# Performance work log

Measured on AMD Instinct MI355X. Metric: run time of the kernel, lower is better.

## Reference

```python
import jax, jax.numpy as jnp
import numpy as np

N_STATE = 1024
N_HEAD = 16
HEAD_DIM = N_STATE // N_HEAD


def setup_inputs() -> dict:
    key = jax.random.key(0)
    ks = jax.random.split(key, 8)
    B, S = 8, 1500
    x = jax.random.normal(ks[0], (B, S, N_STATE), dtype=jnp.float32)
    # additive causal mask (0 on/below diagonal, -inf above), broadcast over B,H
    neg = jnp.float32(-1e9)
    mask = jnp.where(jnp.tril(jnp.ones((S, S), dtype=bool)), 0.0, neg).astype(jnp.float32)
    s = 0.02
    Wq = jax.random.normal(ks[1], (N_STATE, N_STATE), dtype=jnp.float32) * s
    bq = jnp.zeros((N_STATE,), dtype=jnp.float32)
    Wk = jax.random.normal(ks[2], (N_STATE, N_STATE), dtype=jnp.float32) * s
    Wv = jax.random.normal(ks[3], (N_STATE, N_STATE), dtype=jnp.float32) * s
    bv = jnp.zeros((N_STATE,), dtype=jnp.float32)
    Wo = jax.random.normal(ks[4], (N_STATE, N_STATE), dtype=jnp.float32) * s
    bo = jnp.zeros((N_STATE,), dtype=jnp.float32)
    return {"x": x, "mask": mask, "Wq": Wq, "bq": bq, "Wk": Wk, "Wv": Wv, "bv": bv, "Wo": Wo, "bo": bo}


def reference(x, mask, Wq, bq, Wk, Wv, bv, Wo, bo):
    B, S, _ = x.shape
    # linear projections (torch Linear: x @ W^T + b); W stored as [out, in]
    q = x @ Wq.T + bq
    k = x @ Wk.T
    v = x @ Wv.T + bv
    # [B, H, S, D]
    q = q.reshape(B, S, N_HEAD, HEAD_DIM).transpose(0, 2, 1, 3)
    k = k.reshape(B, S, N_HEAD, HEAD_DIM).transpose(0, 2, 1, 3)
    v = v.reshape(B, S, N_HEAD, HEAD_DIM).transpose(0, 2, 1, 3)
    scale = 1.0 / np.sqrt(HEAD_DIM).astype(np.float32)
    scores = jnp.einsum('bhqd,bhkd->bhqk', q, k) * scale + mask
    attn = jax.nn.softmax(scores, axis=-1)
    out = jnp.einsum('bhqk,bhkd->bhqd', attn, v)
    out = out.transpose(0, 2, 1, 3).reshape(B, S, N_STATE)
    return out @ Wo.T + bo
```

## Files before the change

### kernel.cpp

```cpp
#include <hip/hip_runtime.h>
#include <hip/hip_bf16.h>

#define N_STATE 1024
#define N_HEAD  16
#define D_HEAD  64
#define BATCH   8
#define SEQ     1500
#define ROWS    (BATCH*SEQ)
#define SVP     1536
#define MTILES  94

#define BM 128
#define BN 128
#define BK 32

typedef __bf16 bf16x8 __attribute__((ext_vector_type(8)));
typedef __bf16 bf16x4 __attribute__((ext_vector_type(4)));
typedef float  f32x4  __attribute__((ext_vector_type(4)));

__device__ __forceinline__ f32x4 mfma16(bf16x8 a, bf16x8 b, f32x4 c) {
  return __builtin_amdgcn_mfma_f32_16x16x32_bf16(a, b, c, 0, 0, 0);
}

__device__ __forceinline__ void gl_lds16(const void* g, void* l) {
  __builtin_amdgcn_global_load_lds(
      (const __attribute__((address_space(1))) unsigned int*)g,
      (__attribute__((address_space(3))) unsigned int*)l, 16, 0, 0);
}

__global__ __launch_bounds__(256)
void cvt_all(const float* __restrict__ x,  const float* __restrict__ wq,
             const float* __restrict__ wk, const float* __restrict__ wv,
             const float* __restrict__ wo,
             __bf16* __restrict__ xb, __bf16* __restrict__ wb)
{
  const int which = blockIdx.y;
  const float* src;
  __bf16* dst;
  size_t n;
  if (which == 0) { src = x; dst = xb; n = (size_t)ROWS * N_STATE; }
  else {
    src = (which == 1) ? wq : (which == 2) ? wk : (which == 3) ? wv : wo;
    dst = wb + (size_t)(which - 1) * N_STATE * N_STATE;
    n = (size_t)N_STATE * N_STATE;
  }
  const size_t stride = (size_t)gridDim.x * 256 * 4;
  for (size_t i = ((size_t)blockIdx.x * 256 + threadIdx.x) * 4; i < n; i += stride) {
    const f32x4 v = *(const f32x4*)(src + i);
    bf16x4 c; c[0]=(__bf16)v[0]; c[1]=(__bf16)v[1]; c[2]=(__bf16)v[2]; c[3]=(__bf16)v[3];
    *(bf16x4*)(dst + i) = c;
  }
}

__global__ __launch_bounds__(256)
void qkv_fast(const __bf16* __restrict__ xb, const __bf16* __restrict__ wb,
              const float* __restrict__ bq, const float* __restrict__ bv,
              __bf16* __restrict__ q_ws, __bf16* __restrict__ k_ws,
              __bf16* __restrict__ vt_ws)
{
  const int xcd = blockIdx.x & 7;
  const int jj  = blockIdx.x >> 3;
  const int nt  = jj & 7;
  const int mt  = (jj >> 3) * 8 + xcd;
  if (mt >= MTILES) return;

  __shared__ __bf16 lA[BM * BK];
  __shared__ __bf16 lB[BN * BK];
  const int which = blockIdx.z;
  const __bf16* W = wb + (size_t)which * N_STATE * N_STATE;

  const int tid = threadIdx.x;
  const int lane = tid & 63, wave = tid >> 6;
  const int l15 = lane & 15, quad = lane >> 4;
  const int wr = wave >> 1, wc = wave & 1;

  f32x4 acc[4][4] = {};

  for (int k0 = 0; k0 < N_STATE; k0 += BK) {
#pragma unroll
    for (int t = 0; t < 2; ++t) {
      const int c = wave * 2 + t;
      const int s = c * 64 + lane;
      const int row = s >> 2;
      const int sw  = (lane & 3) ^ ((row >> 1) & 3);
      const int ga = min(mt * BM + row, ROWS - 1);
      gl_lds16(xb + (size_t)ga * N_STATE + k0 + sw * 8, (__bf16*)lA + c * 512);
      const int gb = nt * BN + row;
      gl_lds16(W + (size_t)gb * N_STATE + k0 + sw * 8, (__bf16*)lB + c * 512);
    }
    __syncthreads();
    bf16x8 af[4], bfr[4];
#pragma unroll
    for (int i = 0; i < 4; ++i) {
      const int ra = wr * 64 + i * 16 + l15;
      const int rb = wc * 64 + i * 16 + l15;
      af[i]  = *(const bf16x8*)&lA[ra * BK + ((quad ^ ((ra >> 1) & 3)) * 8)];
      bfr[i] = *(const bf16x8*)&lB[rb * BK + ((quad ^ ((rb >> 1) & 3)) * 8)];
    }
    if (which != 2) {
#pragma unroll
      for (int i = 0; i < 4; ++i)
#pragma unroll
        for (int j = 0; j < 4; ++j)
          acc[i][j] = mfma16(af[i], bfr[j], acc[i][j]);
    } else {
#pragma unroll
      for (int i = 0; i < 4; ++i)
#pragma unroll
        for (int j = 0; j < 4; ++j)
          acc[i][j] = mfma16(bfr[j], af[i], acc[i][j]);
    }
    __syncthreads();
  }

  if (which != 2) {
#pragma unroll
    for (int i = 0; i < 4; ++i) {
      const int mrow = mt * BM + wr * 64 + i * 16 + quad * 4;
#pragma unroll
      for (int j = 0; j < 4; ++j) {
        const int col = nt * BN + wc * 64 + j * 16 + l15;
        const int h = col >> 6, d = col & 63;
        const float badd = (which == 0) ? bq[col] : 0.0f;
        __bf16* dst = (which == 0) ? q_ws : k_ws;
#pragma unroll
        for (int r = 0; r < 4; ++r) {
          const int row = mrow + r;
          if (row < ROWS) {
            const int b = row / SEQ, s = row % SEQ;
            dst[(((size_t)(b * N_HEAD + h)) * SEQ + s) * D_HEAD + d] =
                (__bf16)(acc[i][j][r] + badd);
          }
        }
      }
    }
  } else {
#pragma unroll
    for (int i = 0; i < 4; ++i) {
      const int sg = mt * BM + wr * 64 + i * 16 + l15;
      const bool valid = sg < ROWS;
      const int b = sg / SEQ, srow = sg % SEQ;
#pragma unroll
      for (int j = 0; j < 4; ++j) {
        const int dbase = nt * BN + wc * 64 + j * 16 + quad * 4;
#pragma unroll
        for (int r = 0; r < 4; ++r) {
          const int d = dbase + r;
          const int h = d >> 6, dd = d & 63;
          if (valid)
            vt_ws[(((size_t)(b * N_HEAD + h)) * D_HEAD + dd) * SVP + srow] =
                (__bf16)(acc[i][j][r] + bv[d]);
        }
      }
    }
  }
}

__global__ __launch_bounds__(256)
void out_fast(const __bf16* __restrict__ a_in, const __bf16* __restrict__ wob,
              const float* __restrict__ bo, float* __restrict__ out)
{
  const int xcd = blockIdx.x & 7;
  const int jj  = blockIdx.x >> 3;
  const int nt  = jj & 7;
  const int mt  = (jj >> 3) * 8 + xcd;
  if (mt >= MTILES) return;

  __shared__ __bf16 lA[BM * BK];
  __shared__ __bf16 lB[BN * BK];
  const int tid = threadIdx.x;
  const int lane = tid & 63, wave = tid >> 6;
  const int l15 = lane & 15, quad = lane >> 4;
  const int wr = wave >> 1, wc = wave & 1;

  f32x4 acc[4][4] = {};

  for (int k0 = 0; k0 < N_STATE; k0 += BK) {
#pragma unroll
    for (int t = 0; t < 2; ++t) {
      const int c = wave * 2 + t;
      const int s = c * 64 + lane;
      const int row = s >> 2;
      const int sw  = (lane & 3) ^ ((row >> 1) & 3);
      const int ga = min(mt * BM + row, ROWS - 1);
      gl_lds16(a_in + (size_t)ga * N_STATE + k0 + sw * 8, (__bf16*)lA + c * 512);
      const int gb = nt * BN + row;
      gl_lds16(wob + (size_t)gb * N_STATE + k0 + sw * 8, (__bf16*)lB + c * 512);
    }
    __syncthreads();
    bf16x8 af[4], bfr[4];
#pragma unroll
    for (int i = 0; i < 4; ++i) {
      const int ra = wr * 64 + i * 16 + l15;
      const int rb = wc * 64 + i * 16 + l15;
      af[i]  = *(const bf16x8*)&lA[ra * BK + ((quad ^ ((ra >> 1) & 3)) * 8)];
      bfr[i] = *(const bf16x8*)&lB[rb * BK + ((quad ^ ((rb >> 1) & 3)) * 8)];
    }
#pragma unroll
    for (int i = 0; i < 4; ++i)
#pragma unroll
      for (int j = 0; j < 4; ++j)
        acc[i][j] = mfma16(af[i], bfr[j], acc[i][j]);
    __syncthreads();
  }

#pragma unroll
  for (int i = 0; i < 4; ++i) {
    const int mrow = mt * BM + wr * 64 + i * 16 + quad * 4;
#pragma unroll
    for (int j = 0; j < 4; ++j) {
      const int col = nt * BN + wc * 64 + j * 16 + l15;
      const float badd = bo[col];
#pragma unroll
      for (int r = 0; r < 4; ++r) {
        const int row = mrow + r;
        if (row < ROWS)
          out[(size_t)row * N_STATE + col] = acc[i][j][r] + badd;
      }
    }
  }
}

__global__ __launch_bounds__(256)
void qkv_gemm(const float* __restrict__ x,
              const float* __restrict__ Wq, const float* __restrict__ bq,
              const float* __restrict__ Wk,
              const float* __restrict__ Wv, const float* __restrict__ bv,
              __bf16* __restrict__ q_ws, __bf16* __restrict__ k_ws,
              __bf16* __restrict__ vt_ws)
{
  __shared__ __bf16 lA[BM * BK];
  __shared__ __bf16 lB[BN * BK];
  const int which = blockIdx.z;
  const float* W    = (which == 0) ? Wq : (which == 1) ? Wk : Wv;
  const float* bias = (which == 0) ? bq : (which == 2) ? bv : nullptr;

  const int mt = blockIdx.x, nt = blockIdx.y;
  const int tid = threadIdx.x;
  const int lane = tid & 63, wave = tid >> 6;
  const int l15 = lane & 15, quad = lane >> 4;
  const int wr = wave >> 1, wc = wave & 1;

  f32x4 acc[4][4] = {};

  for (int k0 = 0; k0 < N_STATE; k0 += BK) {
#pragma unroll
    for (int it = 0; it < 4; ++it) {
      const int s = tid + it * 256;
      const int row = s >> 3, seg = s & 7;
      const int ga = min(mt * BM + row, ROWS - 1);
      const f32x4 va = *(const f32x4*)(x + (size_t)ga * N_STATE + k0 + seg * 4);
      bf16x4 ca; ca[0]=(__bf16)va[0]; ca[1]=(__bf16)va[1];
                 ca[2]=(__bf16)va[2]; ca[3]=(__bf16)va[3];
      *(bf16x4*)&lA[row * BK + seg * 4] = ca;
      const int gb = nt * BM + row;
      const f32x4 vb = *(const f32x4*)(W + (size_t)gb * N_STATE + k0 + seg * 4);
      bf16x4 cb; cb[0]=(__bf16)vb[0]; cb[1]=(__bf16)vb[1];
                 cb[2]=(__bf16)vb[2]; cb[3]=(__bf16)vb[3];
      *(bf16x4*)&lB[row * BK + seg * 4] = cb;
    }
    __syncthreads();
    bf16x8 af[4], bfr[4];
#pragma unroll
    for (int i = 0; i < 4; ++i) {
      af[i]  = *(const bf16x8*)&lA[(wr * 64 + i * 16 + l15) * BK + quad * 8];
      bfr[i] = *(const bf16x8*)&lB[(wc * 64 + i * 16 + l15) * BK + quad * 8];
    }
    if (which != 2) {
#pragma unroll
      for (int i = 0; i < 4; ++i)
#pragma unroll
        for (int j = 0; j < 4; ++j)
          acc[i][j] = mfma16(af[i], bfr[j], acc[i][j]);
    } else {
#pragma unroll
      for (int i = 0; i < 4; ++i)
#pragma unroll
        for (int j = 0; j < 4; ++j)
          acc[i][j] = mfma16(bfr[j], af[i], acc[i][j]);
    }
    __syncthreads();
  }

  if (which != 2) {
#pragma unroll
    for (int i = 0; i < 4; ++i) {
      const int mrow = mt * BM + wr * 64 + i * 16 + quad * 4;
#pragma unroll
      for (int j = 0; j < 4; ++j) {
        const int col = nt * BN + wc * 64 + j * 16 + l15;
        const int h = col >> 6, d = col & 63;
        const float badd = bias ? bias[col] : 0.0f;
        __bf16* dst = (which == 0) ? q_ws : k_ws;
#pragma unroll
        for (int r = 0; r < 4; ++r) {
          const int row = mrow + r;
          if (row < ROWS) {
            const int b = row / SEQ, s = row % SEQ;
            dst[(((size_t)(b * N_HEAD + h)) * SEQ + s) * D_HEAD + d] =
                (__bf16)(acc[i][j][r] + badd);
          }
        }
      }
    }
  } else {
#pragma unroll
    for (int i = 0; i < 4; ++i) {
      const int sg = mt * BM + wr * 64 + i * 16 + l15;
      const bool valid = sg < ROWS;
      const int b = sg / SEQ, srow = sg % SEQ;
#pragma unroll
      for (int j = 0; j < 4; ++j) {
        const int dbase = nt * BN + wc * 64 + j * 16 + quad * 4;
#pragma unroll
        for (int r = 0; r < 4; ++r) {
          const int d = dbase + r;
          const int h = d >> 6, dd = d & 63;
          if (valid)
            vt_ws[(((size_t)(b * N_HEAD + h)) * D_HEAD + dd) * SVP + srow] =
                (__bf16)(acc[i][j][r] + bias[d]);
        }
      }
    }
  }
}

__global__ __launch_bounds__(256)
void flash_attn(const __bf16* __restrict__ q_ws, const __bf16* __restrict__ k_ws,
                const __bf16* __restrict__ vt_ws, __bf16* __restrict__ attn)
{
  __shared__ __bf16 lK[64 * 72];
  __shared__ __bf16 lV[64 * 72];
  __shared__ __bf16 lP[4 * 16 * 72];
  const int bh = blockIdx.x;
  const int qt = gridDim.y - 1 - blockIdx.y;
  const int tid = threadIdx.x, lane = tid & 63, wave = tid >> 6;
  const int l15 = lane & 15, quad = lane >> 4;
  const __bf16* Q  = q_ws  + (size_t)bh * SEQ * D_HEAD;
  const __bf16* K  = k_ws  + (size_t)bh * SEQ * D_HEAD;
  const __bf16* Vt = vt_ws + (size_t)bh * D_HEAD * SVP;
  __bf16* lPw = lP + wave * 16 * 72;

  const int q0 = qt * 64, wq0 = q0 + wave * 16;
  const int qload = min(wq0 + l15, SEQ - 1);
  const bf16x8 qa0 = *(const bf16x8*)(Q + (size_t)qload * D_HEAD + quad * 8);
  const bf16x8 qa1 = *(const bf16x8*)(Q + (size_t)qload * D_HEAD + 32 + quad * 8);

  const float NEG = -1.0e30f;
  const float scale = 0.125f;
  f32x4 o[4] = {};
  float m_i[4], l_i[4];
#pragma unroll
  for (int r = 0; r < 4; ++r) { m_i[r] = NEG; l_i[r] = 0.0f; }

  const int kmax = min(q0 + 63, SEQ - 1);
  const int wqmax = wq0 + 15;

  for (int kt = 0; kt <= kmax; kt += 64) {
#pragma unroll
    for (int it = 0; it < 2; ++it) {
      const int s = tid + it * 256;
      const int row = s >> 3, seg = s & 7;
      const int gk = min(kt + row, SEQ - 1);
      *(bf16x8*)&lK[row * 72 + seg * 8] =
          *(const bf16x8*)(K + (size_t)gk * D_HEAD + seg * 8);
      *(bf16x8*)&lV[row * 72 + seg * 8] =
          *(const bf16x8*)(Vt + (size_t)row * SVP + kt + seg * 8);
    }
    __syncthreads();

    if (kt <= wqmax) {
      f32x4 sg[4] = {};
#pragma unroll
      for (int g = 0; g < 4; ++g) {
        const __bf16* kr = &lK[(g * 16 + l15) * 72 + quad * 8];
        sg[g] = mfma16(qa0, *(const bf16x8*)kr, sg[g]);
        sg[g] = mfma16(qa1, *(const bf16x8*)(kr + 32), sg[g]);
      }
      const bool fullvis = (kt + 63 <= wq0) && (kt + 63 < SEQ);
      float alpha[4];
#pragma unroll
      for (int r = 0; r < 4; ++r) {
        const int qr = wq0 + quad * 4 + r;
        float v[4];
        if (fullvis) {
#pragma unroll
          for (int g = 0; g < 4; ++g) v[g] = sg[g][r] * scale;
        } else {
#pragma unroll
          for (int g = 0; g < 4; ++g) {
            const int krow = kt + g * 16 + l15;
            v[g] = (krow <= qr && krow < SEQ) ? sg[g][r] * scale : NEG;
          }
        }
        float tmax = fmaxf(fmaxf(v[0], v[1]), fmaxf(v[2], v[3]));
#pragma unroll
        for (int off = 1; off < 16; off <<= 1)
          tmax = fmaxf(tmax, __shfl_xor(tmax, off));
        const float mnew = fmaxf(m_i[r], tmax);
        alpha[r] = __expf(m_i[r] - mnew);
        float e[4], rsum = 0.0f;
#pragma unroll
        for (int g = 0; g < 4; ++g) { e[g] = __expf(v[g] - mnew); rsum += e[g]; }
#pragma unroll
        for (int off = 1; off < 16; off <<= 1)
          rsum += __shfl_xor(rsum, off);
        l_i[r] = l_i[r] * alpha[r] + rsum;
        m_i[r] = mnew;
#pragma unroll
        for (int g = 0; g < 4; ++g)
          lPw[(quad * 4 + r) * 72 + g * 16 + l15] = (__bf16)e[g];
      }
#pragma unroll
      for (int nn = 0; nn < 4; ++nn)
#pragma unroll
        for (int r = 0; r < 4; ++r) o[nn][r] *= alpha[r];

#pragma unroll
      for (int h = 0; h < 2; ++h) {
        const bf16x8 pa = *(const bf16x8*)&lPw[l15 * 72 + h * 32 + quad * 8];
#pragma unroll
        for (int nn = 0; nn < 4; ++nn) {
          const bf16x8 vb =
              *(const bf16x8*)&lV[(nn * 16 + l15) * 72 + h * 32 + quad * 8];
          o[nn] = mfma16(pa, vb, o[nn]);
        }
      }
    }
    __syncthreads();
  }

  const int b = bh >> 4, h = bh & 15;
#pragma unroll
  for (int r = 0; r < 4; ++r) {
    const int qr = wq0 + quad * 4 + r;
    if (qr < SEQ) {
      const float inv = 1.0f / l_i[r];
#pragma unroll
      for (int nn = 0; nn < 4; ++nn) {
        attn[(((size_t)(b * SEQ + qr)) * N_HEAD + h) * D_HEAD + nn * 16 + l15] =
            (__bf16)(o[nn][r] * inv);
      }
    }
  }
}

__global__ __launch_bounds__(256)
void out_gemm(const __bf16* __restrict__ a_in, const float* __restrict__ Wo,
              const float* __restrict__ bo, float* __restrict__ out)
{
  __shared__ __bf16 lA[BM * BK];
  __shared__ __bf16 lB[BN * BK];
  const int mt = blockIdx.x, nt = blockIdx.y;
  const int tid = threadIdx.x;
  const int lane = tid & 63, wave = tid >> 6;
  const int l15 = lane & 15, quad = lane >> 4;
  const int wr = wave >> 1, wc = wave & 1;

  f32x4 acc[4][4] = {};

  for (int k0 = 0; k0 < N_STATE; k0 += BK) {
#pragma unroll
    for (int it = 0; it < 2; ++it) {
      const int s = tid + it * 256;
      const int row = s >> 2, seg = s & 3;
      const int ga = min(mt * BM + row, ROWS - 1);
      *(bf16x8*)&lA[row * BK + seg * 8] =
          *(const bf16x8*)(a_in + (size_t)ga * N_STATE + k0 + seg * 8);
    }
#pragma unroll
    for (int it = 0; it < 4; ++it) {
      const int s = tid + it * 256;
      const int row = s >> 3, seg = s & 7;
      const int gb = nt * BM + row;
      const f32x4 vb = *(const f32x4*)(Wo + (size_t)gb * N_STATE + k0 + seg * 4);
      bf16x4 cb; cb[0]=(__bf16)vb[0]; cb[1]=(__bf16)vb[1];
                 cb[2]=(__bf16)vb[2]; cb[3]=(__bf16)vb[3];
      *(bf16x4*)&lB[row * BK + seg * 4] = cb;
    }
    __syncthreads();
    bf16x8 af[4], bfr[4];
#pragma unroll
    for (int i = 0; i < 4; ++i) {
      af[i]  = *(const bf16x8*)&lA[(wr * 64 + i * 16 + l15) * BK + quad * 8];
      bfr[i] = *(const bf16x8*)&lB[(wc * 64 + i * 16 + l15) * BK + quad * 8];
    }
#pragma unroll
    for (int i = 0; i < 4; ++i)
#pragma unroll
      for (int j = 0; j < 4; ++j)
        acc[i][j] = mfma16(af[i], bfr[j], acc[i][j]);
    __syncthreads();
  }

#pragma unroll
  for (int i = 0; i < 4; ++i) {
    const int mrow = mt * BM + wr * 64 + i * 16 + quad * 4;
#pragma unroll
    for (int j = 0; j < 4; ++j) {
      const int col = nt * BN + wc * 64 + j * 16 + l15;
      const float badd = bo[col];
#pragma unroll
      for (int r = 0; r < 4; ++r) {
        const int row = mrow + r;
        if (row < ROWS)
          out[(size_t)row * N_STATE + col] = acc[i][j][r] + badd;
      }
    }
  }
}

extern "C" void kernel_launch(void* const* d_in, const int* in_sizes, int n_in,
                              void* d_out, int out_size, void* d_ws, size_t ws_size,
                              hipStream_t stream) {
  const float* x  = (const float*)d_in[0];
  const float* Wq = (const float*)d_in[2];
  const float* bq = (const float*)d_in[3];
  const float* Wk = (const float*)d_in[4];
  const float* Wv = (const float*)d_in[5];
  const float* bv = (const float*)d_in[6];
  const float* Wo = (const float*)d_in[7];
  const float* bo = (const float*)d_in[8];
  float* out = (float*)d_out;

  const size_t chunk  = (size_t)ROWS * N_STATE;
  const size_t vchunk = (size_t)BATCH * N_HEAD * D_HEAD * SVP;
  const size_t wchunk = (size_t)4 * N_STATE * N_STATE;
  __bf16* q_ws  = (__bf16*)d_ws;
  __bf16* k_ws  = q_ws + chunk;
  __bf16* vt_ws = k_ws + chunk;
  __bf16* attn  = vt_ws + vchunk;
  __bf16* xb    = attn;
  __bf16* wb    = attn + chunk;
  const size_t need = (3 * chunk + vchunk + wchunk) * sizeof(__bf16);

  const int MT = (ROWS + BM - 1) / BM;
  if (ws_size >= need) {
    cvt_all<<<dim3(1024, 5), 256, 0, stream>>>(x, Wq, Wk, Wv, Wo, xb, wb);
    qkv_fast<<<dim3(768, 1, 3), 256, 0, stream>>>(
        xb, wb, bq, bv, q_ws, k_ws, vt_ws);
    flash_attn<<<dim3(BATCH * N_HEAD, (SEQ + 63) / 64), 256, 0, stream>>>(
        q_ws, k_ws, vt_ws, attn);
    out_fast<<<dim3(768, 1, 1), 256, 0, stream>>>(
        attn, wb + (size_t)3 * N_STATE * N_STATE, bo, out);
  } else {
    qkv_gemm<<<dim3(MT, N_STATE / BN, 3), 256, 0, stream>>>(
        x, Wq, bq, Wk, Wv, bv, q_ws, k_ws, vt_ws);
    flash_attn<<<dim3(BATCH * N_HEAD, (SEQ + 63) / 64), 256, 0, stream>>>(
        q_ws, k_ws, vt_ws, attn);
    out_gemm<<<dim3(MT, N_STATE / BN), 256, 0, stream>>>(attn, Wo, bo, out);
  }
}
```

Measured before the change: 421.6 us.

## Transpose attention MFMAs so each lane owns a query row, load K/V via direct LDS

The flash-attention kernel swaps MFMA operand order so S^T and O^T are computed, giving each lane a single query column. Softmax max and sum then need only two cross-quad shuffles instead of four-step reductions per row, and the per-row state collapses to one scalar. K/V tiles are loaded into a chunked LDS layout with direct global-to-LDS loads instead of register round-trips. P is written as packed bf16x4 and the output is stored as vectorised bf16x4, at the cost of a new LDS layout whose bank-conflict behaviour is untested.

Measured after the change: 381.9 us. 9.4% less time.

```diff
diff --git a/kernel.cpp b/kernel.cpp
--- a/kernel.cpp
+++ b/kernel.cpp
@@ -329,9 +329,9 @@
 void flash_attn(const __bf16* __restrict__ q_ws, const __bf16* __restrict__ k_ws,
                 const __bf16* __restrict__ vt_ws, __bf16* __restrict__ attn)
 {
-  __shared__ __bf16 lK[64 * 72];
-  __shared__ __bf16 lV[64 * 72];
-  __shared__ __bf16 lP[4 * 16 * 72];
+  __shared__ __align__(16) __bf16 lK[8 * 512];
+  __shared__ __align__(16) __bf16 lV[8 * 512];
+  __shared__ __align__(16) __bf16 lP[4 * 16 * 72];
   const int bh = blockIdx.x;
   const int qt = gridDim.y - 1 - blockIdx.y;
   const int tid = threadIdx.x, lane = tid & 63, wave = tid >> 6;
@@ -348,24 +348,20 @@
 
   const float NEG = -1.0e30f;
   const float scale = 0.125f;
+  const int query = wq0 + l15;
   f32x4 o[4] = {};
-  float m_i[4], l_i[4];
-#pragma unroll
-  for (int r = 0; r < 4; ++r) { m_i[r] = NEG; l_i[r] = 0.0f; }
+  float m_i = NEG, l_i = 0.0f;
 
   const int kmax = min(q0 + 63, SEQ - 1);
   const int wqmax = wq0 + 15;
 
   for (int kt = 0; kt <= kmax; kt += 64) {
 #pragma unroll
-    for (int it = 0; it < 2; ++it) {
-      const int s = tid + it * 256;
-      const int row = s >> 3, seg = s & 7;
-      const int gk = min(kt + row, SEQ - 1);
-      *(bf16x8*)&lK[row * 72 + seg * 8] =
-          *(const bf16x8*)(K + (size_t)gk * D_HEAD + seg * 8);
-      *(bf16x8*)&lV[row * 72 + seg * 8] =
-          *(const bf16x8*)(Vt + (size_t)row * SVP + kt + seg * 8);
+    for (int t = 0; t < 2; ++t) {
+      const int c = wave * 2 + t;
+      const int gk = min(kt + lane, SEQ - 1);
+      gl_lds16(K + (size_t)gk * D_HEAD + c * 8, (__bf16*)lK + c * 512);
+      gl_lds16(Vt + (size_t)lane * SVP + kt + c * 8, (__bf16*)lV + c * 512);
     }
     __syncthreads();
 
@@ -373,74 +369,74 @@
       f32x4 sg[4] = {};
 #pragma unroll
       for (int g = 0; g < 4; ++g) {
-        const __bf16* kr = &lK[(g * 16 + l15) * 72 + quad * 8];
-        sg[g] = mfma16(qa0, *(const bf16x8*)kr, sg[g]);
-        sg[g] = mfma16(qa1, *(const bf16x8*)(kr + 32), sg[g]);
+        const bf16x8 k0 = *(const bf16x8*)&lK[quad * 512 + (g * 16 + l15) * 8];
+        const bf16x8 k1 = *(const bf16x8*)&lK[(4 + quad) * 512 + (g * 16 + l15) * 8];
+        sg[g] = mfma16(k0, qa0, sg[g]);
+        sg[g] = mfma16(k1, qa1, sg[g]);
       }
       const bool fullvis = (kt + 63 <= wq0) && (kt + 63 < SEQ);
-      float alpha[4];
-#pragma unroll
-      for (int r = 0; r < 4; ++r) {
-        const int qr = wq0 + quad * 4 + r;
-        float v[4];
-        if (fullvis) {
-#pragma unroll
-          for (int g = 0; g < 4; ++g) v[g] = sg[g][r] * scale;
-        } else {
-#pragma unroll
-          for (int g = 0; g < 4; ++g) {
-            const int krow = kt + g * 16 + l15;
-            v[g] = (krow <= qr && krow < SEQ) ? sg[g][r] * scale : NEG;
+      float tmax = NEG;
+#pragma unroll
+      for (int g = 0; g < 4; ++g)
+#pragma unroll
+        for (int r = 0; r < 4; ++r) {
+          float v = sg[g][r] * scale;
+          if (!fullvis) {
+            const int key = kt + g * 16 + quad * 4 + r;
+            v = (key <= query && key < SEQ) ? v : NEG;
           }
-        }
-        float tmax = fmaxf(fmaxf(v[0], v[1]), fmaxf(v[2], v[3]));
-#pragma unroll
-        for (int off = 1; off < 16; off <<= 1)
-          tmax = fmaxf(tmax, __shfl_xor(tmax, off));
-        const float mnew = fmaxf(m_i[r], tmax);
-        alpha[r] = __expf(m_i[r] - mnew);
-        float e[4], rsum = 0.0f;
-#pragma unroll
-        for (int g = 0; g < 4; ++g) { e[g] = __expf(v[g] - mnew); rsum += e[g]; }
-#pragma unroll
-        for (int off = 1; off < 16; off <<= 1)
-          rsum += __shfl_xor(rsum, off);
-        l_i[r] = l_i[r] * alpha[r] + rsum;
-        m_i[r] = mnew;
-#pragma unroll
-        for (int g = 0; g < 4; ++g)
-          lPw[(quad * 4 + r) * 72 + g * 16 + l15] = (__bf16)e[g];
-      }
+          sg[g][r] = v;
+          tmax = fmaxf(tmax, v);
+        }
+      tmax = fmaxf(tmax, __shfl_xor(tmax, 16));
+      tmax = fmaxf(tmax, __shfl_xor(tmax, 32));
+      const float mnew = fmaxf(m_i, tmax);
+      const float alpha = __expf(m_i - mnew);
+      float rsum = 0.0f;
+#pragma unroll
+      for (int g = 0; g < 4; ++g) {
+        bf16x4 pk;
+#pragma unroll
+        for (int r = 0; r < 4; ++r) {
+          const float e = __expf(sg[g][r] - mnew);
+          rsum += e;
+          pk[r] = (__bf16)e;
+        }
+        *(bf16x4*)&lPw[l15 * 72 + g * 16 + quad * 4] = pk;
+      }
+      rsum += __shfl_xor(rsum, 16);
+      rsum += __shfl_xor(rsum, 32);
+      l_i = l_i * alpha + rsum;
+      m_i = mnew;
 #pragma unroll
       for (int nn = 0; nn < 4; ++nn)
 #pragma unroll
-        for (int r = 0; r < 4; ++r) o[nn][r] *= alpha[r];
+        for (int r = 0; r < 4; ++r) o[nn][r] *= alpha;
 
 #pragma unroll
       for (int h = 0; h < 2; ++h) {
-        const bf16x8 pa = *(const bf16x8*)&lPw[l15 * 72 + h * 32 + quad * 8];
+        const bf16x8 pb = *(const bf16x8*)&lPw[l15 * 72 + h * 32 + quad * 8];
 #pragma unroll
         for (int nn = 0; nn < 4; ++nn) {
-          const bf16x8 vb =
-              *(const bf16x8*)&lV[(nn * 16 + l15) * 72 + h * 32 + quad * 8];
-          o[nn] = mfma16(pa, vb, o[nn]);
-        }
-      }
-    }
-    __syncthreads();
-  }
-
-  const int b = bh >> 4, h = bh & 15;
-#pragma unroll
-  for (int r = 0; r < 4; ++r) {
-    const int qr = wq0 + quad * 4 + r;
-    if (qr < SEQ) {
-      const float inv = 1.0f / l_i[r];
-#pragma unroll
-      for (int nn = 0; nn < 4; ++nn) {
-        attn[(((size_t)(b * SEQ + qr)) * N_HEAD + h) * D_HEAD + nn * 16 + l15] =
-            (__bf16)(o[nn][r] * inv);
-      }
+          const bf16x8 va =
+              *(const bf16x8*)&lV[(h * 4 + quad) * 512 + (nn * 16 + l15) * 8];
+          o[nn] = mfma16(va, pb, o[nn]);
+        }
+      }
+    }
+    __syncthreads();
+  }
+
+  const int b = bh >> 4, hh = bh & 15;
+  if (query < SEQ) {
+    const float inv = 1.0f / l_i;
+#pragma unroll
+    for (int nn = 0; nn < 4; ++nn) {
+      bf16x4 ov;
+#pragma unroll
+      for (int r = 0; r < 4; ++r) ov[r] = (__bf16)(o[nn][r] * inv);
+      *(bf16x4*)&attn[(((size_t)(b * SEQ + query)) * N_HEAD + hh) * D_HEAD +
+                      nn * 16 + quad * 4] = ov;
     }
   }
 }
```
